# Performance work log

Hardware: AMD Instinct MI355X
Metric: run time of the kernel (lower is better)

The kernel has to match this reference:

```python
import jax, jax.numpy as jnp
import numpy as np

BN_EPS = 1e-5


def binarize(x):
    # sign binarization with straight-through estimator (identity grad)
    return x + jax.lax.stop_gradient(jnp.sign(x) - x)


def conv2d(x, w, stride):
    # x: [N,C,H,W], w: [O,I,kh,kw], VALID padding (PyTorch default padding=0)
    return jax.lax.conv_general_dilated(
        x, w, window_strides=(stride, stride), padding='VALID',
        dimension_numbers=('NCHW', 'OIHW', 'NCHW'))


def batchnorm(x, gamma, beta, mean, var):
    inv = gamma / jnp.sqrt(var + BN_EPS)          # [C]
    return x * inv[None, :, None, None] + (beta - mean * inv)[None, :, None, None]


def setup_inputs() -> dict:
    key = jax.random.key(0)
    ks = jax.random.split(key, 20)
    B = 8192
    f32 = jnp.float32
    d = {
        'x': jax.random.normal(ks[0], (B, 1, 24, 54), f32),
        'conv1_w': jax.random.normal(ks[1], (32, 1, 3, 3), f32) * 0.3,
        'conv1_b': jax.random.normal(ks[2], (32,), f32) * 0.1,
        'bn1_gamma': 1.0 + 0.1 * jax.random.normal(ks[3], (32,), f32),
        'bn1_beta': 0.1 * jax.random.normal(ks[4], (32,), f32),
        'bn1_mean': 0.1 * jax.random.normal(ks[5], (32,), f32),
        'bn1_var': jax.random.uniform(ks[6], (32,), f32, 0.5, 1.5),
        'conv2_w': jax.random.normal(ks[7], (64, 32, 3, 3), f32) * 0.1,
        'conv2_b': jax.random.normal(ks[8], (64,), f32) * 0.1,
        'bn2_gamma': 1.0 + 0.1 * jax.random.normal(ks[9], (64,), f32),
        'bn2_beta': 0.1 * jax.random.normal(ks[10], (64,), f32),
        'bn2_mean': 0.1 * jax.random.normal(ks[11], (64,), f32),
        'bn2_var': jax.random.uniform(ks[12], (64,), f32, 0.5, 1.5),
        'lin_w': jax.random.normal(ks[13], (500, 3840), f32) * 0.02,
        'lin_b': jax.random.normal(ks[14], (500,), f32) * 0.1,
        'out_w': jax.random.normal(ks[15], (10, 500), f32) * 0.05,
        'out_b': jax.random.normal(ks[16], (10,), f32) * 0.1,
    }
    return d


def reference(x, conv1_w, conv1_b, bn1_gamma, bn1_beta, bn1_mean, bn1_var,
              conv2_w, conv2_b, bn2_gamma, bn2_beta, bn2_mean, bn2_var,
              lin_w, lin_b, out_w, out_b):
    # conv1: input channels (1) != 3 -> input binarized; weight binarized; float bias
    h = conv2d(binarize(x), binarize(conv1_w), 2) + conv1_b[None, :, None, None]
    h = jax.nn.relu(batchnorm(h, bn1_gamma, bn1_beta, bn1_mean, bn1_var))  # [B,32,11,26]
    # conv2: input channels (32) != 3 -> input binarized (values in {0,1} post-ReLU)
    h = conv2d(binarize(h), binarize(conv2_w), 2) + conv2_b[None, :, None, None]
    h = jax.nn.relu(batchnorm(h, bn2_gamma, bn2_beta, bn2_mean, bn2_var))  # [B,64,5,12]
    h = h.reshape(-1, 3840)
    # BinarizeLinear: in_features (3840, 500) != 784 -> input binarized
    h = jax.nn.relu(binarize(h) @ binarize(lin_w).T + lin_b[None, :])      # [B,500]
    y = binarize(h) @ binarize(out_w).T + out_b[None, :]                   # [B,10]
    return y
```

## Files before the change

kernel.cpp:

```cpp
#include <hip/hip_runtime.h>
#include <cstdint>

#define BN_EPS 1e-5f

static constexpr int NB = 8192;
static constexpr int JLIN = 500;


__global__ __launch_bounds__(256) void pack_kernel(
    const float* __restrict__ conv1_w, const float* __restrict__ conv1_b,
    const float* __restrict__ conv2_w, const float* __restrict__ conv2_b,
    const float* __restrict__ lin_w, const float* __restrict__ lin_b,
    const float* __restrict__ out_w,
    const float* __restrict__ bn1_g, const float* __restrict__ bn1_b,
    const float* __restrict__ bn1_m, const float* __restrict__ bn1_v,
    const float* __restrict__ bn2_g, const float* __restrict__ bn2_b,
    const float* __restrict__ bn2_m, const float* __restrict__ bn2_v,
    uint32_t* __restrict__ wlin4, uint32_t* __restrict__ cdat,
    uint32_t* __restrict__ lut, uint32_t* __restrict__ wout,
    int* __restrict__ Tlin)
{
    __shared__ uint32_t s_bm[122];
    __shared__ float    s_c1w[288];
    __shared__ uint32_t s_wp[32];
    __shared__ float    s_inv1[32], s_sh1[32], s_b1[32];

    int tid  = threadIdx.x;
    int lane = tid & 63;
    int wv   = tid >> 6;
    int b    = blockIdx.x;

    if (b < 500) {
        int j = b;
        if (tid == 0) { s_bm[120] = 0; s_bm[121] = 0; }
        for (int it = 0; it < 15; ++it) {
            int i = it * 256 + tid;
            float v = lin_w[(size_t)j * 3840 + i];
            uint64_t mask = __ballot(v > 0.0f);
            if (lane == 0)
                *((uint64_t*)&s_bm[(it * 256 + wv * 64) >> 5]) = mask;
        }
        __syncthreads();
        if (tid < 128) {
            int k = tid;
            int c = k >> 1, hi = k & 1;
            int nb = hi ? 28 : 32;
            int f0 = c * 60 + hi * 32;
            uint32_t lo  = s_bm[f0 >> 5];
            uint32_t hiw = s_bm[(f0 >> 5) + 1];
            int sh = f0 & 31;
            uint32_t word = (uint32_t)((((uint64_t)hiw << 32) | lo) >> sh);
            if (nb < 32) word &= (1u << nb) - 1u;
            int jw = j >> 6, jl = j & 63, kq = k >> 2, q = k & 3;
            wlin4[jw * 8192 + kq * 256 + jl * 4 + q] = word;
        }
        return;
    }

    int mb = b - 500;
    if (mb < 2) {
        for (int i = tid; i < 288; i += 256) s_c1w[i] = conv1_w[i];
        __syncthreads();
        if (tid < 32) {
            uint32_t wp = 0;
            for (int t = 0; t < 9; ++t)
                wp |= (s_c1w[tid * 9 + t] < 0.0f ? 1u : 0u) << t;
            s_wp[tid] = wp;
            float inv = bn1_g[tid] / sqrtf(bn1_v[tid] + BN_EPS);
            s_inv1[tid] = inv;
            s_sh1[tid]  = bn1_b[tid] - bn1_m[tid] * inv;
            s_b1[tid]   = conv1_b[tid];
        }
        __syncthreads();
        uint32_t px = (uint32_t)(mb * 256 + tid);
        uint32_t word = 0;
        for (int c = 0; c < 32; ++c) {
            int d = 9 - 2 * __popc(px ^ s_wp[c]);
            float z = __fadd_rn((float)d, s_b1[c]);
            z = __fadd_rn(__fmul_rn(z, s_inv1[c]), s_sh1[c]);
            word |= (z > 0.0f ? 1u : 0u) << c;
        }
        lut[px] = word;
        return;
    }

    int idx = (mb - 2) * 256 + tid;
    if (idx < 576) {
        int c = idx / 9, tap = idx % 9;
        uint32_t w = 0;
        for (int ic = 0; ic < 32; ++ic)
            w |= (conv2_w[c * 288 + ic * 9 + tap] > 0.0f ? 1u : 0u) << ic;
        float inv = bn2_g[c] / sqrtf(bn2_v[c] + BN_EPS);
        if (inv < 0.0f) w = ~w;
        cdat[c * 10 + tap] = w;
    } else if (idx < 576 + 64) {
        int c = idx - 576;
        float inv = bn2_g[c] / sqrtf(bn2_v[c] + BN_EPS);
        float sh  = bn2_b[c] - bn2_m[c] * inv;
        float b2  = conv2_b[c];
        int T = 10000;
        for (int u = -300; u <= 300; ++u) {
            float v = (inv < 0.0f) ? (float)(-u) : (float)u;
            float z = __fadd_rn(__fmul_rn(__fadd_rn(v, b2), inv), sh);
            if (z > 0.0f) { T = u; break; }
        }
        cdat[c * 10 + 9] = (uint32_t)T;
    } else if (idx < 576 + 64 + 512) {
        int j = idx - (576 + 64);
        int T = 10000;
        if (j < JLIN) {
            float lb = lin_b[j];
            int base = (int)floorf(-lb) - 2;
            for (int u = base; u <= base + 5; ++u)
                if (__fadd_rn((float)u, lb) > 0.0f) { T = u; break; }
        }
        Tlin[j] = T;
    } else if (idx < 576 + 64 + 512 + 160) {
        int t = idx - (576 + 64 + 512);
        int j = t >> 4, k = t & 15;
        uint32_t w = 0;
        for (int bb = 0; bb < 32; ++bb) {
            int jj = k * 32 + bb;
            if (jj < JLIN) w |= (out_w[j * 500 + jj] > 0.0f ? 1u : 0u) << bb;
        }
        wout[t] = w;
    }
}

__global__ __launch_bounds__(256, 6) void conv_kernel(
    const float* __restrict__ x,
    const uint32_t* __restrict__ cdat,
    const uint32_t* __restrict__ lut,
    uint32_t* __restrict__ h2b, int* __restrict__ Bs)
{
    __shared__ uint64_t s_rows[4][24];
    __shared__ uint32_t s_lut[512];
    __shared__ uint32_t s_in[4][288];

    int tid  = threadIdx.x;
    int lane = tid & 63;
    int wv   = tid >> 6;
    int s    = blockIdx.x * 4 + wv;

    s_lut[tid]       = lut[tid];
    s_lut[tid + 256] = lut[tid + 256];

    const float* xs = x + (size_t)s * 1296;
    for (int r = 0; r < 24; ++r) {
        float v = (lane < 54) ? xs[r * 54 + lane] : 1.0f;
        uint64_t mk = __ballot(v < 0.0f);
        if (lane == 0) s_rows[wv][r] = mk;
    }
    __syncthreads();

    for (int i = tid; i < 4 * 286; i += 256) {
        int sl = i / 286, p = i - sl * 286;
        int oy = p / 26, ox = p - oy * 26;
        uint64_t r0 = s_rows[sl][2 * oy];
        uint64_t r1 = s_rows[sl][2 * oy + 1];
        uint64_t r2 = s_rows[sl][2 * oy + 2];
        int sh = 2 * ox;
        uint32_t px = ((uint32_t)(r0 >> sh) & 7u)
                    | (((uint32_t)(r1 >> sh) & 7u) << 3)
                    | (((uint32_t)(r2 >> sh) & 7u) << 6);
        s_in[sl][p] = s_lut[px];
    }
    __syncthreads();

    int p  = (lane < 60) ? lane : 59;
    int oy = p / 12, ox = p - 12 * oy;
    uint32_t t[9];
    #pragma unroll
    for (int ky = 0; ky < 3; ++ky) {
        const uint32_t* rp = &s_in[wv][(2 * oy + ky) * 26 + 2 * ox];
        t[ky * 3 + 0] = rp[0];
        t[ky * 3 + 1] = rp[1];
        t[ky * 3 + 2] = rp[2];
    }
    int B = 0;
    #pragma unroll
    for (int q = 0; q < 9; ++q) B += __popc(t[q]);
    int nB = -B;

    uint32_t w0 = 0, w1 = 0;
    #pragma unroll 4
    for (int c = 0; c < 64; ++c) {
        const uint32_t* cd = cdat + c * 10;
        int P = 0;
        #pragma unroll
        for (int q = 0; q < 9; ++q) P += __popc(t[q] & cd[q]);
        int v = 2 * P + nB;
        uint64_t mk = __ballot(v >= (int)cd[9]);
        if (lane == c) {
            w0 = (uint32_t)mk;
            w1 = (uint32_t)(mk >> 32) & 0x0FFFFFFFu;
        }
    }

    int bsum = __popc(w0) + __popc(w1);
    #pragma unroll
    for (int off = 32; off > 0; off >>= 1) bsum += __shfl_xor(bsum, off, 64);
    if (lane == 0) Bs[s] = bsum;

    *(uint2*)(h2b + (size_t)s * 128 + 2 * lane) = make_uint2(w0, w1);
}

__global__ __launch_bounds__(256) void lin_kernel(
    const uint32_t* __restrict__ h2b,
    const uint32_t* __restrict__ wlin4,
    const int* __restrict__ Tlin,
    const int* __restrict__ Bs,
    uint64_t* __restrict__ h3)
{
    __shared__ uint4 s_w[2048];

    int tid  = threadIdx.x;
    int lane = tid & 63;
    int wv   = __builtin_amdgcn_readfirstlane((int)(tid >> 6));
    int jw    = blockIdx.x >> 7;
    int chunk = blockIdx.x & 127;

    const uint4* wsrc = (const uint4*)wlin4 + (size_t)jw * 2048;
    #pragma unroll
    for (int i = 0; i < 8; ++i)
        s_w[i * 256 + tid] = wsrc[i * 256 + tid];

    int j = jw * 64 + lane;
    int T = Tlin[j];
    int sbase = chunk * 64 + wv * 16;
    __syncthreads();

    int P[16];
    #pragma unroll
    for (int i = 0; i < 16; ++i) P[i] = 0;

    for (int kq = 0; kq < 32; ++kq) {
        uint4 w4 = s_w[kq * 64 + lane];
        const uint4* abase = (const uint4*)(h2b + (size_t)sbase * 128) + kq;
        #pragma unroll
        for (int i = 0; i < 16; ++i) {
            uint4 a = abase[i * 32];
            P[i] += __popc(a.x & w4.x);
            P[i] += __popc(a.y & w4.y);
            P[i] += __popc(a.z & w4.z);
            P[i] += __popc(a.w & w4.w);
        }
    }

    #pragma unroll
    for (int i = 0; i < 16; ++i) {
        int s = sbase + i;
        int v = 2 * P[i] - Bs[s];
        uint64_t mk = __ballot(v >= T);
        if (lane == 0) h3[(size_t)jw * NB + s] = mk;
    }
}

__global__ __launch_bounds__(256) void out_kernel(
    const uint64_t* __restrict__ h3,
    const uint32_t* __restrict__ wout,
    const float* __restrict__ out_b,
    float* __restrict__ out)
{
    int gidx = blockIdx.x * 256 + threadIdx.x;
    int o = gidx >> 13;
    int s = gidx & 8191;
    const uint64_t* wo = (const uint64_t*)wout + o * 8;
    int P = 0, B = 0;
    #pragma unroll
    for (int k = 0; k < 8; ++k) {
        uint64_t a = h3[(size_t)k * NB + s];
        P += __popcll(a & wo[k]);
        B += __popcll(a);
    }
    out[(size_t)s * 10 + o] = __fadd_rn((float)(2 * P - B), out_b[o]);
}

extern "C" void kernel_launch(void* const* d_in, const int* in_sizes, int n_in,
                              void* d_out, int out_size, void* d_ws, size_t ws_size,
                              hipStream_t stream)
{
    const float* x       = (const float*)d_in[0];
    const float* conv1_w = (const float*)d_in[1];
    const float* conv1_b = (const float*)d_in[2];
    const float* bn1_g   = (const float*)d_in[3];
    const float* bn1_b   = (const float*)d_in[4];
    const float* bn1_m   = (const float*)d_in[5];
    const float* bn1_v   = (const float*)d_in[6];
    const float* conv2_w = (const float*)d_in[7];
    const float* conv2_b = (const float*)d_in[8];
    const float* bn2_g   = (const float*)d_in[9];
    const float* bn2_b   = (const float*)d_in[10];
    const float* bn2_m   = (const float*)d_in[11];
    const float* bn2_v   = (const float*)d_in[12];
    const float* lin_w   = (const float*)d_in[13];
    const float* lin_b   = (const float*)d_in[14];
    const float* out_w   = (const float*)d_in[15];
    const float* out_b   = (const float*)d_in[16];

    char* ws = (char*)d_ws;
    uint32_t* h2b   = (uint32_t*)(ws + 0);
    uint64_t* h3    = (uint64_t*)(ws + 4194304);
    uint32_t* wlin4 = (uint32_t*)(ws + 4718592);
    uint32_t* cdat  = (uint32_t*)(ws + 4980736);
    uint32_t* lut   = (uint32_t*)(ws + 4983296);
    uint32_t* wout  = (uint32_t*)(ws + 4985344);
    int*      Tlin  = (int*)     (ws + 4985984);
    int*      Bs    = (int*)     (ws + 4988032);

    pack_kernel<<<508, 256, 0, stream>>>(conv1_w, conv1_b, conv2_w, conv2_b,
                                         lin_w, lin_b, out_w,
                                         bn1_g, bn1_b, bn1_m, bn1_v,
                                         bn2_g, bn2_b, bn2_m, bn2_v,
                                         wlin4, cdat, lut, wout, Tlin);
    conv_kernel<<<NB / 4, 256, 0, stream>>>(x, cdat, lut, h2b, Bs);
    lin_kernel<<<1024, 256, 0, stream>>>(h2b, wlin4, Tlin, Bs, h3);
    out_kernel<<<320, 256, 0, stream>>>(h3, wout, out_b, (float*)d_out);
}
```

Before: 199.0 us.

## Remap conv2 to lane-per-channel, coalesce input load, fuse output layer into linear kernel

The conv kernel now loads each sample's input as a flat coalesced stream of bits instead of row by row. It assigns one lane per output channel, keeping that channel's weights in registers, and reads the shared activation tiles instead of doing 64 ballots per wave. The row-sum term is precomputed in a separate shared pass. The linear kernel now loops over all eight output-neuron groups for 16 samples per block and computes the final 10-way layer in place, which removes the separate output kernel and the h3 round trip. The trade-off is that each block reloads 32 KB of packed weights eight times, and with only 512 blocks and 4 samples per wave, parallelism and weight reuse per load are lower.

```diff
diff --git a/kernel.cpp b/kernel.cpp
--- a/kernel.cpp
+++ b/kernel.cpp
@@ -92,7 +92,7 @@
             w |= (conv2_w[c * 288 + ic * 9 + tap] > 0.0f ? 1u : 0u) << ic;
         float inv = bn2_g[c] / sqrtf(bn2_v[c] + BN_EPS);
         if (inv < 0.0f) w = ~w;
-        cdat[c * 10 + tap] = w;
+        cdat[tap * 64 + c] = w;
     } else if (idx < 576 + 64) {
         int c = idx - 576;
         float inv = bn2_g[c] / sqrtf(bn2_v[c] + BN_EPS);
@@ -104,7 +104,7 @@
             float z = __fadd_rn(__fmul_rn(__fadd_rn(v, b2), inv), sh);
             if (z > 0.0f) { T = u; break; }
         }
-        cdat[c * 10 + 9] = (uint32_t)T;
+        cdat[576 + c] = (uint32_t)T;
     } else if (idx < 576 + 64 + 512) {
         int j = idx - (576 + 64);
         int T = 10000;
@@ -133,9 +133,10 @@
     const uint32_t* __restrict__ lut,
     uint32_t* __restrict__ h2b, int* __restrict__ Bs)
 {
-    __shared__ uint64_t s_rows[4][24];
+    __shared__ __align__(8) uint32_t s_flat[4][44];
     __shared__ uint32_t s_lut[512];
-    __shared__ uint32_t s_in[4][288];
+    __shared__ __align__(8) uint32_t s_in[4][288];
+    __shared__ uint32_t s_base[4][60];
 
     int tid  = threadIdx.x;
     int lane = tid & 63;
@@ -146,54 +147,71 @@
     s_lut[tid + 256] = lut[tid + 256];
 
     const float* xs = x + (size_t)s * 1296;
-    for (int r = 0; r < 24; ++r) {
-        float v = (lane < 54) ? xs[r * 54 + lane] : 1.0f;
+    #pragma unroll
+    for (int it = 0; it < 21; ++it) {
+        int f = it * 64 + lane;
+        float v = (f < 1296) ? xs[f] : 1.0f;
         uint64_t mk = __ballot(v < 0.0f);
-        if (lane == 0) s_rows[wv][r] = mk;
+        if (lane == 0) *((uint64_t*)&s_flat[wv][2 * it]) = mk;
     }
     __syncthreads();
 
     for (int i = tid; i < 4 * 286; i += 256) {
         int sl = i / 286, p = i - sl * 286;
         int oy = p / 26, ox = p - oy * 26;
-        uint64_t r0 = s_rows[sl][2 * oy];
-        uint64_t r1 = s_rows[sl][2 * oy + 1];
-        uint64_t r2 = s_rows[sl][2 * oy + 2];
-        int sh = 2 * ox;
-        uint32_t px = ((uint32_t)(r0 >> sh) & 7u)
-                    | (((uint32_t)(r1 >> sh) & 7u) << 3)
-                    | (((uint32_t)(r2 >> sh) & 7u) << 6);
-        s_in[sl][p] = s_lut[px];
+        uint32_t pxb = 0;
+        #pragma unroll
+        for (int ky = 0; ky < 3; ++ky) {
+            int bitpos = 54 * (2 * oy + ky) + 2 * ox;
+            int d  = bitpos >> 5;
+            int sh = bitpos & 31;
+            uint64_t wp = (uint64_t)s_flat[sl][d] | ((uint64_t)s_flat[sl][d + 1] << 32);
+            pxb |= (((uint32_t)(wp >> sh)) & 7u) << (3 * ky);
+        }
+        s_in[sl][p] = s_lut[pxb];
     }
     __syncthreads();
 
-    int p  = (lane < 60) ? lane : 59;
-    int oy = p / 12, ox = p - 12 * oy;
-    uint32_t t[9];
+    for (int i = tid; i < 4 * 60; i += 256) {
+        int sl = i / 60, p = i - sl * 60;
+        int oy = p / 12, ox = p - 12 * oy;
+        uint32_t sum = 0;
+        #pragma unroll
+        for (int ky = 0; ky < 3; ++ky) {
+            const uint32_t* rp = &s_in[sl][(2 * oy + ky) * 26 + 2 * ox];
+            sum += __popc(rp[0]) + __popc(rp[1]) + __popc(rp[2]);
+        }
+        s_base[sl][p] = sum;
+    }
+    __syncthreads();
+
+    int c = lane;
+    uint32_t m[9];
     #pragma unroll
-    for (int ky = 0; ky < 3; ++ky) {
-        const uint32_t* rp = &s_in[wv][(2 * oy + ky) * 26 + 2 * ox];
-        t[ky * 3 + 0] = rp[0];
-        t[ky * 3 + 1] = rp[1];
-        t[ky * 3 + 2] = rp[2];
-    }
-    int B = 0;
+    for (int q = 0; q < 9; ++q) m[q] = cdat[q * 64 + c];
+    int T = (int)cdat[576 + c];
+
+    uint32_t w0 = 0, w1 = 0;
     #pragma unroll
-    for (int q = 0; q < 9; ++q) B += __popc(t[q]);
-    int nB = -B;
-
-    uint32_t w0 = 0, w1 = 0;
-    #pragma unroll 4
-    for (int c = 0; c < 64; ++c) {
-        const uint32_t* cd = cdat + c * 10;
-        int P = 0;
-        #pragma unroll
-        for (int q = 0; q < 9; ++q) P += __popc(t[q] & cd[q]);
-        int v = 2 * P + nB;
-        uint64_t mk = __ballot(v >= (int)cd[9]);
-        if (lane == c) {
-            w0 = (uint32_t)mk;
-            w1 = (uint32_t)(mk >> 32) & 0x0FFFFFFFu;
+    for (int oy = 0; oy < 5; ++oy) {
+        #pragma unroll
+        for (int ox = 0; ox < 12; ++ox) {
+            const int p = oy * 12 + ox;
+            int P = 0;
+            #pragma unroll
+            for (int ky = 0; ky < 3; ++ky) {
+                const uint32_t* rp = &s_in[wv][(2 * oy + ky) * 26 + 2 * ox];
+                uint64_t ab = *(const uint64_t*)rp;
+                uint32_t t0 = (uint32_t)ab;
+                uint32_t t1 = (uint32_t)(ab >> 32);
+                uint32_t t2 = rp[2];
+                P += __popc(t0 & m[ky * 3 + 0]);
+                P += __popc(t1 & m[ky * 3 + 1]);
+                P += __popc(t2 & m[ky * 3 + 2]);
+            }
+            int v = 2 * P - (int)s_base[wv][p];
+            uint32_t bit = (v >= T) ? 1u : 0u;
+            if (p < 32) w0 |= bit << p; else w1 |= bit << (p - 32);
         }
     }
 
@@ -202,7 +220,7 @@
     for (int off = 32; off > 0; off >>= 1) bsum += __shfl_xor(bsum, off, 64);
     if (lane == 0) Bs[s] = bsum;
 
-    *(uint2*)(h2b + (size_t)s * 128 + 2 * lane) = make_uint2(w0, w1);
+    *(uint2*)(h2b + (size_t)s * 128 + 2 * c) = make_uint2(w0, w1);
 }
 
 __global__ __launch_bounds__(256) void lin_kernel(
@@ -210,70 +228,63 @@
     const uint32_t* __restrict__ wlin4,
     const int* __restrict__ Tlin,
     const int* __restrict__ Bs,
-    uint64_t* __restrict__ h3)
-{
-    __shared__ uint4 s_w[2048];
-
-    int tid  = threadIdx.x;
-    int lane = tid & 63;
-    int wv   = __builtin_amdgcn_readfirstlane((int)(tid >> 6));
-    int jw    = blockIdx.x >> 7;
-    int chunk = blockIdx.x & 127;
-
-    const uint4* wsrc = (const uint4*)wlin4 + (size_t)jw * 2048;
-    #pragma unroll
-    for (int i = 0; i < 8; ++i)
-        s_w[i * 256 + tid] = wsrc[i * 256 + tid];
-
-    int j = jw * 64 + lane;
-    int T = Tlin[j];
-    int sbase = chunk * 64 + wv * 16;
-    __syncthreads();
-
-    int P[16];
-    #pragma unroll
-    for (int i = 0; i < 16; ++i) P[i] = 0;
-
-    for (int kq = 0; kq < 32; ++kq) {
-        uint4 w4 = s_w[kq * 64 + lane];
-        const uint4* abase = (const uint4*)(h2b + (size_t)sbase * 128) + kq;
-        #pragma unroll
-        for (int i = 0; i < 16; ++i) {
-            uint4 a = abase[i * 32];
-            P[i] += __popc(a.x & w4.x);
-            P[i] += __popc(a.y & w4.y);
-            P[i] += __popc(a.z & w4.z);
-            P[i] += __popc(a.w & w4.w);
-        }
-    }
-
-    #pragma unroll
-    for (int i = 0; i < 16; ++i) {
-        int s = sbase + i;
-        int v = 2 * P[i] - Bs[s];
-        uint64_t mk = __ballot(v >= T);
-        if (lane == 0) h3[(size_t)jw * NB + s] = mk;
-    }
-}
-
-__global__ __launch_bounds__(256) void out_kernel(
-    const uint64_t* __restrict__ h3,
     const uint32_t* __restrict__ wout,
     const float* __restrict__ out_b,
     float* __restrict__ out)
 {
-    int gidx = blockIdx.x * 256 + threadIdx.x;
-    int o = gidx >> 13;
-    int s = gidx & 8191;
-    const uint64_t* wo = (const uint64_t*)wout + o * 8;
-    int P = 0, B = 0;
-    #pragma unroll
-    for (int k = 0; k < 8; ++k) {
-        uint64_t a = h3[(size_t)k * NB + s];
-        P += __popcll(a & wo[k]);
-        B += __popcll(a);
-    }
-    out[(size_t)s * 10 + o] = __fadd_rn((float)(2 * P - B), out_b[o]);
+    __shared__ uint4    s_w[2048];
+    __shared__ uint64_t s_h3[16][8];
+    __shared__ uint64_t s_wout[10][8];
+
+    int tid  = threadIdx.x;
+    int lane = tid & 63;
+    int wv   = __builtin_amdgcn_readfirstlane((int)(tid >> 6));
+    int sbase = blockIdx.x * 16;
+
+    if (tid < 80) ((uint64_t*)s_wout)[tid] = ((const uint64_t*)wout)[tid];
+
+    for (int jw = 0; jw < 8; ++jw) {
+        const uint4* wsrc = (const uint4*)wlin4 + (size_t)jw * 2048;
+        #pragma unroll
+        for (int i = 0; i < 8; ++i)
+            s_w[i * 256 + tid] = wsrc[i * 256 + tid];
+        int T = Tlin[jw * 64 + lane];
+        __syncthreads();
+
+        int smp = sbase + wv * 4;
+        int P[4] = {0, 0, 0, 0};
+        #pragma unroll 4
+        for (int kq = 0; kq < 32; ++kq) {
+            uint4 w4 = s_w[kq * 64 + lane];
+            #pragma unroll
+            for (int i = 0; i < 4; ++i) {
+                uint4 a = *((const uint4*)(h2b + (size_t)(smp + i) * 128) + kq);
+                P[i] += __popc(a.x & w4.x);
+                P[i] += __popc(a.y & w4.y);
+                P[i] += __popc(a.z & w4.z);
+                P[i] += __popc(a.w & w4.w);
+            }
+        }
+        #pragma unroll
+        for (int i = 0; i < 4; ++i) {
+            int v = 2 * P[i] - Bs[smp + i];
+            uint64_t mk = __ballot(v >= T);
+            if (lane == 0) s_h3[wv * 4 + i][jw] = mk;
+        }
+        __syncthreads();
+    }
+
+    if (tid < 160) {
+        int sl = tid / 10, o = tid - sl * 10;
+        int P = 0, B = 0;
+        #pragma unroll
+        for (int k = 0; k < 8; ++k) {
+            uint64_t a = s_h3[sl][k];
+            P += __popcll(a & s_wout[o][k]);
+            B += __popcll(a);
+        }
+        out[(size_t)(sbase + sl) * 10 + o] = __fadd_rn((float)(2 * P - B), out_b[o]);
+    }
 }
 
 extern "C" void kernel_launch(void* const* d_in, const int* in_sizes, int n_in,
@@ -300,7 +311,6 @@
 
     char* ws = (char*)d_ws;
     uint32_t* h2b   = (uint32_t*)(ws + 0);
-    uint64_t* h3    = (uint64_t*)(ws + 4194304);
     uint32_t* wlin4 = (uint32_t*)(ws + 4718592);
     uint32_t* cdat  = (uint32_t*)(ws + 4980736);
     uint32_t* lut   = (uint32_t*)(ws + 4983296);
@@ -314,6 +324,6 @@
                                          bn2_g, bn2_b, bn2_m, bn2_v,
                                          wlin4, cdat, lut, wout, Tlin);
     conv_kernel<<<NB / 4, 256, 0, stream>>>(x, cdat, lut, h2b, Bs);
-    lin_kernel<<<1024, 256, 0, stream>>>(h2b, wlin4, Tlin, Bs, h3);
-    out_kernel<<<320, 256, 0, stream>>>(h3, wout, out_b, (float*)d_out);
+    lin_kernel<<<512, 256, 0, stream>>>(h2b, wlin4, Tlin, Bs, wout, out_b,
+                                        (float*)d_out);
 }
```

Result: slower. 278.1 us (+39.8%).
